# Performance work log

Measured on AMD Instinct MI355X. Metric: run time of the kernel, lower is better.

The kernel has to match this reference:

```python
import jax, jax.numpy as jnp
import numpy as np

DIM = 96
SHIFT_SIZE = 3
EPS = 1e-5


def conv1x1(x, w, b):
    # x: [B,C,H,W], w: [O,C], b: [O]
    return jnp.einsum('bchw,oc->bohw', x, w) + b[None, :, None, None]


def group_norm1(x, gamma, beta):
    # GroupNorm with 1 group: normalize over (C,H,W) per sample
    mean = jnp.mean(x, axis=(1, 2, 3), keepdims=True)
    var = jnp.var(x, axis=(1, 2, 3), keepdims=True)
    xn = (x - mean) * jax.lax.rsqrt(var + EPS)
    return xn * gamma[None, :, None, None] + beta[None, :, None, None]


def axial_shift(x, shift_size, axis, sign=1):
    # pad -> chunk channels -> roll each chunk -> cat -> narrow (zero-fill shift)
    B, C, H, W = x.shape
    p = shift_size // 2
    xp = jnp.pad(x, ((0, 0), (0, 0), (p, p), (p, p)))
    chunks = jnp.split(xp, shift_size, axis=1)
    rolled = [jnp.roll(c, sign * s, axis=axis) for c, s in zip(chunks, range(-p, p + 1))]
    xc = jnp.concatenate(rolled, axis=1)
    return xc[:, :, p:p + H, p:p + W]


def setup_inputs() -> dict:
    key = jax.random.key(0)
    ks = jax.random.split(key, 13)
    B, C, H, W = 4, DIM, 256, 256
    s = 1.0 / np.sqrt(C)
    inp = {
        'x': jax.random.normal(ks[0], (B, C, H, W), jnp.float32),
        'w1': jax.random.uniform(ks[1], (C, C), jnp.float32, -s, s),
        'b1': jax.random.uniform(ks[2], (C,), jnp.float32, -s, s),
        'w21': jax.random.uniform(ks[3], (C, C), jnp.float32, -s, s),
        'b21': jax.random.uniform(ks[4], (C,), jnp.float32, -s, s),
        'w22': jax.random.uniform(ks[5], (C, C), jnp.float32, -s, s),
        'b22': jax.random.uniform(ks[6], (C,), jnp.float32, -s, s),
        'w3': jax.random.uniform(ks[7], (C, C), jnp.float32, -s, s),
        'b3': jax.random.uniform(ks[8], (C,), jnp.float32, -s, s),
        'gn1_w': jnp.ones((C,), jnp.float32),
        'gn1_b': jnp.zeros((C,), jnp.float32),
        'gn2_w': jnp.ones((C,), jnp.float32),
        'gn2_b': jnp.zeros((C,), jnp.float32),
    }
    return inp


def reference(x, w1, b1, w21, b21, w22, b22, w3, b3, gn1_w, gn1_b, gn2_w, gn2_b):
    gelu = lambda t: jax.nn.gelu(t, approximate=False)  # torch nn.GELU default (erf)
    x = gelu(group_norm1(conv1x1(x, w1, b1), gn1_w, gn1_b))
    x_lr = axial_shift(x, SHIFT_SIZE, axis=3)
    x_l_diag = axial_shift(x_lr, SHIFT_SIZE, axis=2)
    x_td = axial_shift(x, SHIFT_SIZE, axis=2)
    x_r_diag = axial_shift(x_td, SHIFT_SIZE, axis=3, sign=-1)
    out = (gelu(conv1x1(x_lr, w21, b21)) + gelu(conv1x1(x_l_diag, w21, b21))
           + gelu(conv1x1(x_td, w22, b22)) + gelu(conv1x1(x_r_diag, w22, b22)))
    out = group_norm1(out, gn2_w, gn2_b)
    return conv1x1(out, w3, b3)
```

## Files before the change

### kernel.cpp

```cpp
#include <hip/hip_runtime.h>
#include <hip/hip_bf16.h>
#include <math.h>


#define B_ 4
#define C_ 96
#define H_ 256
#define W_ 256
#define NPIX (H_ * W_)
#define GN_N ((float)(C_ * NPIX))
#define CPAD 104

#define HT 8
#define WT 16
#define HHT (HT + 2)
#define HWT (WT + 2)
#define HALO_PX (HHT * HWT)
#define GR_PX 12
#define ROW_GR (HWT * GR_PX)
#define TOT_GR (HHT * ROW_GR)

typedef __attribute__((ext_vector_type(4))) float f32x4;
typedef __attribute__((ext_vector_type(8))) short short8;
typedef __attribute__((ext_vector_type(2))) unsigned int uint2v;

__device__ __forceinline__ unsigned short f2bf(float v) {
    unsigned int u = __float_as_uint(v);
    unsigned int r = (u + 0x7FFFu + ((u >> 16) & 1u)) >> 16;
    return (unsigned short)r;
}
__device__ __forceinline__ float bf2f(unsigned short u) {
    return __uint_as_float(((unsigned int)u) << 16);
}

__device__ __forceinline__ float gelu_f(float v) {
    float t = fmaf(v * v, 0.07135481627f, 1.5957691216f);
    float e = __expf(v * t);
    float r = __builtin_amdgcn_rcpf(e + 1.0f);
    return v - v * r;
}

__device__ __forceinline__ float waveReduceSum(float v) {
#pragma unroll
    for (int off = 32; off > 0; off >>= 1) v += __shfl_down(v, off);
    return v;
}

__device__ __forceinline__ f32x4 mfma16(short8 a, short8 b, f32x4 c) {
    return __builtin_amdgcn_mfma_f32_16x16x32_bf16(a, b, c, 0, 0, 0);
}

__global__ void k0_prep(const float* __restrict__ w1, const float* __restrict__ w21,
                        const float* __restrict__ w22, const float* __restrict__ w3,
                        unsigned short* __restrict__ wb, float* __restrict__ stats) {
    int t = blockIdx.x * 256 + threadIdx.x;
    if (blockIdx.x == 0 && threadIdx.x < 16) stats[threadIdx.x] = 0.f;
    if (t >= 4 * C_ * C_) return;
    int m = t / (C_ * C_);
    int r = t - m * (C_ * C_);
    const float* src = (m == 0) ? w1 : (m == 1) ? w21 : (m == 2) ? w22 : w3;
    wb[t] = f2bf(src[r]);
}

__global__ __launch_bounds__(256, 3) void k1_conv1(
    const float* __restrict__ x, const unsigned short* __restrict__ w1b,
    const float* __restrict__ b1, unsigned short* __restrict__ ap,
    float* __restrict__ stats) {
    __shared__ unsigned short xs[256 * CPAD];
    __shared__ float red[8];
    int tid = threadIdx.x;
    int b = blockIdx.x >> 8;
    int h = blockIdx.x & 255;
    int pix0 = h << 8;
    size_t xbase = (size_t)b * C_ * NPIX + pix0 + tid;
    int lb = tid * CPAD;
#pragma unroll
    for (int c0 = 0; c0 < C_; c0 += 8) {
        short8 pk;
#pragma unroll
        for (int j = 0; j < 8; ++j)
            pk[j] = (short)f2bf(x[xbase + (size_t)(c0 + j) * NPIX]);
        *reinterpret_cast<short8*>(&xs[lb + c0]) = pk;
    }
    __syncthreads();
    int l = tid & 63, wv = tid >> 6;
    int bx = l & 15, q = l >> 4, cl = q * 8;
    short8 bfr[4][3];
#pragma unroll
    for (int nf = 0; nf < 4; ++nf) {
        int p = (4 * wv + nf) * 16 + bx;
#pragma unroll
        for (int kb = 0; kb < 3; ++kb)
            bfr[nf][kb] = *reinterpret_cast<const short8*>(&xs[p * CPAD + kb * 32 + cl]);
    }
    unsigned int* xsu = reinterpret_cast<unsigned int*>(xs);
    float ls = 0.f, lsq = 0.f;
    for (int mt = 0; mt < 6; ++mt) {
        int m0 = mt * 16;
        const unsigned short* wp = w1b + (m0 + bx) * C_ + cl;
        short8 af[3];
#pragma unroll
        for (int kb = 0; kb < 3; ++kb)
            af[kb] = *reinterpret_cast<const short8*>(wp + kb * 32);
        f32x4 acc[4];
#pragma unroll
        for (int nf = 0; nf < 4; ++nf) acc[nf] = (f32x4){0.f, 0.f, 0.f, 0.f};
#pragma unroll
        for (int nf = 0; nf < 4; ++nf)
#pragma unroll
            for (int kb = 0; kb < 3; ++kb)
                acc[nf] = mfma16(af[kb], bfr[nf][kb], acc[nf]);
        int o = m0 + q * 4;
        float b0 = b1[o], b1v = b1[o + 1], b2v = b1[o + 2], b3v = b1[o + 3];
#pragma unroll
        for (int nf = 0; nf < 4; ++nf) {
            int p = (4 * wv + nf) * 16 + bx;
            float y0 = acc[nf][0] + b0, y1v = acc[nf][1] + b1v;
            float y2 = acc[nf][2] + b2v, y3 = acc[nf][3] + b3v;
            ls += y0 + y1v + y2 + y3;
            lsq += y0 * y0 + y1v * y1v + y2 * y2 + y3 * y3;
            xsu[p * (CPAD / 2) + (o >> 1)] =
                (unsigned int)f2bf(y0) | ((unsigned int)f2bf(y1v) << 16);
            xsu[p * (CPAD / 2) + (o >> 1) + 1] =
                (unsigned int)f2bf(y2) | ((unsigned int)f2bf(y3) << 16);
        }
    }
    __syncthreads();
    size_t abase = (size_t)(b * NPIX + pix0 + tid) * C_;
#pragma unroll
    for (int c0 = 0; c0 < C_; c0 += 8)
        *reinterpret_cast<short8*>(&ap[abase + c0]) =
            *reinterpret_cast<short8*>(&xs[tid * CPAD + c0]);
    ls = waveReduceSum(ls);
    lsq = waveReduceSum(lsq);
    if (l == 0) { red[wv] = ls; red[4 + wv] = lsq; }
    __syncthreads();
    if (tid == 0) {
        atomicAdd(&stats[b], red[0] + red[1] + red[2] + red[3]);
        atomicAdd(&stats[4 + b], red[4] + red[5] + red[6] + red[7]);
    }
}

__global__ void k2_fin(float* stats, int so, int dof) {
    int t = threadIdx.x;
    if (t < 4) {
        float mean = stats[so + t] / GN_N;
        float var = stats[so + 4 + t] / GN_N - mean * mean;
        stats[dof + t] = mean;
        stats[dof + 4 + t] = rsqrtf(var + 1e-5f);
    }
}

__global__ __launch_bounds__(256, 4) void k3_main(
    const unsigned short* __restrict__ ap,
    const unsigned short* __restrict__ w21b, const float* __restrict__ b21,
    const unsigned short* __restrict__ w22b, const float* __restrict__ b22,
    const float* __restrict__ gn1w, const float* __restrict__ gn1b,
    unsigned short* __restrict__ zb, float* __restrict__ stats) {
    __shared__ unsigned short as_t[HALO_PX * CPAD];
    __shared__ float red[8];
    __shared__ float scs[C_], offs[C_];
    int tid = threadIdx.x;
    int wseg = blockIdx.x & 15;
    int hseg = (blockIdx.x >> 4) & 31;
    int b = blockIdx.x >> 9;
    int l = tid & 63, wv = tid >> 6;
    int h0 = hseg * HT, w0 = wseg * WT;
    float m1 = stats[16 + b], r1 = stats[20 + b];
    if (tid < C_) {
        float sc = r1 * gn1w[tid];
        scs[tid] = sc;
        offs[tid] = gn1b[tid] - m1 * sc;
    }
    __syncthreads();
    for (int g = tid; g < TOT_GR; g += 256) {
        int row = g / ROW_GR;
        int rem = g - row * ROW_GR;
        int p = rem / GR_PX;
        int cgr = rem - p * GR_PX;
        int hh = h0 - 1 + row, ww = w0 - 1 + p;
        bool valid = ((unsigned)hh < (unsigned)H_) && ((unsigned)ww < (unsigned)W_);
        int hc = valid ? hh : 0, wc = valid ? ww : 0;
        short8 raw = *reinterpret_cast<const short8*>(
            &ap[(size_t)(b * NPIX + hc * W_ + wc) * C_ + cgr * 8]);
        short8 pk;
#pragma unroll
        for (int j = 0; j < 8; ++j) {
            int c = cgr * 8 + j;
            float f = bf2f((unsigned short)raw[j]);
            float gv = gelu_f(fmaf(f, scs[c], offs[c]));
            pk[j] = valid ? (short)f2bf(gv) : (short)0;
        }
        *reinterpret_cast<short8*>(&as_t[(row * HWT + p) * CPAD + cgr * 8]) = pk;
    }
    __syncthreads();
    int bx = l & 15, q = l >> 4, cl = q * 8;
    int Xb = (bx + 1) * CPAD + cl;
#define FR(R, dx, kb) (*reinterpret_cast<const short8*>( \
        &as_t[((R)*HWT + (dx)) * CPAD + Xb + (kb)*32]))
    float ls = 0.f, lsq = 0.f;
#pragma unroll
    for (int nf = 0; nf < 2; ++nf) {
        int r = 2 * wv + nf;
        short8 f0a = FR(r + 1, 1, 0), f0b = FR(r + 2, 1, 0);
        short8 f0c = FR(r + 2, 0, 0), f0d = FR(r + 2, -1, 0);
        short8 fC = FR(r + 1, 0, 1);
        short8 f2a = FR(r + 1, -1, 2), f2b = FR(r, -1, 2);
        short8 f2c = FR(r, 0, 2), f2d = FR(r, 1, 2);
        size_t zpix = (size_t)(b * NPIX + (h0 + r) * W_ + w0 + bx) * C_;
        for (int mt = 0; mt < 6; ++mt) {
            int m0 = mt * 16;
            const unsigned short* wpa = w21b + (m0 + bx) * C_ + cl;
            const unsigned short* wpb = w22b + (m0 + bx) * C_ + cl;
            short8 aA0 = *reinterpret_cast<const short8*>(wpa);
            short8 aA1 = *reinterpret_cast<const short8*>(wpa + 32);
            short8 aA2 = *reinterpret_cast<const short8*>(wpa + 64);
            short8 aB0 = *reinterpret_cast<const short8*>(wpb);
            short8 aB1 = *reinterpret_cast<const short8*>(wpb + 32);
            short8 aB2 = *reinterpret_cast<const short8*>(wpb + 64);
            f32x4 a0 = (f32x4){0.f, 0.f, 0.f, 0.f}, a1 = a0, a2 = a0, a3 = a0;
            a0 = mfma16(aA0, f0a, a0);
            a1 = mfma16(aA0, f0b, a1);
            a2 = mfma16(aB0, f0c, a2);
            a3 = mfma16(aB0, f0d, a3);
            a0 = mfma16(aA1, fC, a0);
            a1 = mfma16(aA1, fC, a1);
            a2 = mfma16(aB1, fC, a2);
            a3 = mfma16(aB1, fC, a3);
            a0 = mfma16(aA2, f2a, a0);
            a1 = mfma16(aA2, f2b, a1);
            a2 = mfma16(aB2, f2c, a2);
            a3 = mfma16(aB2, f2d, a3);
            const f32x4 bb1 = *reinterpret_cast<const f32x4*>(&b21[m0 + q * 4]);
            const f32x4 bb2 = *reinterpret_cast<const f32x4*>(&b22[m0 + q * 4]);
            float zv[4];
#pragma unroll
            for (int rg = 0; rg < 4; ++rg) {
                float z0 = gelu_f(a0[rg] + bb1[rg]) + gelu_f(a1[rg] + bb1[rg]) +
                           gelu_f(a2[rg] + bb2[rg]) + gelu_f(a3[rg] + bb2[rg]);
                zv[rg] = z0;
                ls += z0;
                lsq += z0 * z0;
            }
            uint2v pk;
            pk.x = (unsigned int)f2bf(zv[0]) | ((unsigned int)f2bf(zv[1]) << 16);
            pk.y = (unsigned int)f2bf(zv[2]) | ((unsigned int)f2bf(zv[3]) << 16);
            *reinterpret_cast<uint2v*>(&zb[zpix + m0 + q * 4]) = pk;
        }
    }
#undef FR
    ls = waveReduceSum(ls);
    lsq = waveReduceSum(lsq);
    if (l == 0) { red[wv] = ls; red[4 + wv] = lsq; }
    __syncthreads();
    if (tid == 0) {
        atomicAdd(&stats[8 + b], red[0] + red[1] + red[2] + red[3]);
        atomicAdd(&stats[12 + b], red[4] + red[5] + red[6] + red[7]);
    }
}

__global__ __launch_bounds__(256, 3) void k5_conv3(
    const unsigned short* __restrict__ zb,
    const unsigned short* __restrict__ w3b, const float* __restrict__ b3,
    const float* __restrict__ gn2w, const float* __restrict__ gn2b,
    float* __restrict__ out, const float* __restrict__ stats) {
    __shared__ unsigned short zs[256 * CPAD];
    __shared__ float scs[C_], offs[C_];
    int tid = threadIdx.x;
    int b = blockIdx.x >> 8;
    int pix0 = (blockIdx.x & 255) << 8;
    float m2 = stats[24 + b], r2 = stats[28 + b];
    if (tid < C_) {
        float sc = r2 * gn2w[tid];
        scs[tid] = sc;
        offs[tid] = gn2b[tid] - m2 * sc;
    }
    __syncthreads();
    {
        const short8* src = reinterpret_cast<const short8*>(
            &zb[(size_t)(b * NPIX + pix0 + tid) * C_]);
        int lb = tid * CPAD;
#pragma unroll
        for (int i = 0; i < 12; ++i) {
            short8 v = src[i];
            short8 pk;
#pragma unroll
            for (int j = 0; j < 8; ++j) {
                int c = i * 8 + j;
                pk[j] = (short)f2bf(fmaf(bf2f((unsigned short)v[j]), scs[c], offs[c]));
            }
            *reinterpret_cast<short8*>(&zs[lb + i * 8]) = pk;
        }
    }
    __syncthreads();
    int l = tid & 63, wv = tid >> 6;
    int bx = l & 15, q = l >> 4, cl = q * 8;
    short8 bfr[4][3];
#pragma unroll
    for (int nf = 0; nf < 4; ++nf) {
        int p = (4 * wv + nf) * 16 + bx;
#pragma unroll
        for (int kb = 0; kb < 3; ++kb)
            bfr[nf][kb] = *reinterpret_cast<const short8*>(&zs[p * CPAD + kb * 32 + cl]);
    }
    for (int mt = 0; mt < 6; ++mt) {
        int m0 = mt * 16;
        const unsigned short* wp = w3b + (m0 + bx) * C_ + cl;
        short8 af[3];
#pragma unroll
        for (int kb = 0; kb < 3; ++kb)
            af[kb] = *reinterpret_cast<const short8*>(wp + kb * 32);
        f32x4 acc[4];
#pragma unroll
        for (int nf = 0; nf < 4; ++nf) acc[nf] = (f32x4){0.f, 0.f, 0.f, 0.f};
#pragma unroll
        for (int nf = 0; nf < 4; ++nf)
#pragma unroll
            for (int kb = 0; kb < 3; ++kb)
                acc[nf] = mfma16(af[kb], bfr[nf][kb], acc[nf]);
        int o = m0 + q * 4;
        float b0 = b3[o], b1v = b3[o + 1], b2v = b3[o + 2], b3v = b3[o + 3];
#pragma unroll
        for (int nf = 0; nf < 4; ++nf) {
            int p = pix0 + (4 * wv + nf) * 16 + bx;
            size_t ob0 = (size_t)(b * C_ + o) * NPIX + p;
            out[ob0] = acc[nf][0] + b0;
            out[ob0 + NPIX] = acc[nf][1] + b1v;
            out[ob0 + 2 * NPIX] = acc[nf][2] + b2v;
            out[ob0 + 3 * NPIX] = acc[nf][3] + b3v;
        }
    }
}

extern "C" void kernel_launch(void* const* d_in, const int* in_sizes, int n_in,
                              void* d_out, int out_size, void* d_ws, size_t ws_size,
                              hipStream_t stream) {
    const float* x = (const float*)d_in[0];
    const float* w1 = (const float*)d_in[1];
    const float* b1 = (const float*)d_in[2];
    const float* w21 = (const float*)d_in[3];
    const float* b21 = (const float*)d_in[4];
    const float* w22 = (const float*)d_in[5];
    const float* b22 = (const float*)d_in[6];
    const float* w3 = (const float*)d_in[7];
    const float* b3 = (const float*)d_in[8];
    const float* gn1w = (const float*)d_in[9];
    const float* gn1b = (const float*)d_in[10];
    const float* gn2w = (const float*)d_in[11];
    const float* gn2b = (const float*)d_in[12];
    float* out = (float*)d_out;
    char* ws = (char*)d_ws;

    const size_t NB = (size_t)B_ * NPIX * C_ * sizeof(unsigned short);
    unsigned short* ap = (unsigned short*)ws;
    unsigned short* zb = (unsigned short*)(ws + NB);
    float* stats = (float*)(ws + 2 * NB);
    unsigned short* wb = (unsigned short*)(ws + 2 * NB + 128);
    unsigned short* w1b = wb;
    unsigned short* w21b = wb + C_ * C_;
    unsigned short* w22b = wb + 2 * C_ * C_;
    unsigned short* w3b = wb + 3 * C_ * C_;

    hipLaunchKernelGGL(k0_prep, dim3(144), dim3(256), 0, stream,
                       w1, w21, w22, w3, wb, stats);
    hipLaunchKernelGGL(k1_conv1, dim3(1024), dim3(256), 0, stream, x, w1b, b1, ap, stats);
    hipLaunchKernelGGL(k2_fin, dim3(1), dim3(64), 0, stream, stats, 0, 16);
    hipLaunchKernelGGL(k3_main, dim3(2048), dim3(256), 0, stream,
                       ap, w21b, b21, w22b, b22, gn1w, gn1b, zb, stats);
    hipLaunchKernelGGL(k2_fin, dim3(1), dim3(64), 0, stream, stats, 8, 24);
    hipLaunchKernelGGL(k5_conv3, dim3(1024), dim3(256), 0, stream,
                       zb, w3b, b3, gn2w, gn2b, out, stats);
}
```

Before: 170.1 us.

## Split GN1+GELU into own pass, drop LDS halo, fold GN2 into conv3 weights

GroupNorm1 affine plus GELU moves out of the shifted-conv kernel into a separate in-place pass over the activation buffer. The main kernel then reads its shifted fragments straight from global memory with per-load bounds masking instead of staging a halo tile in LDS. That removes the halo recompute of GELU and the LDS footprint, but costs an extra full read/write pass over the activations. GroupNorm2 is folded into per-batch conv3 weights and biases by a tiny kernel, so conv3 loads B fragments directly without LDS normalization. GELU now uses exp2 with pre-scaled constants.

```diff
diff --git a/kernel.cpp b/kernel.cpp
--- a/kernel.cpp
+++ b/kernel.cpp
@@ -11,15 +11,6 @@
 #define GN_N ((float)(C_ * NPIX))
 #define CPAD 104
 
-#define HT 8
-#define WT 16
-#define HHT (HT + 2)
-#define HWT (WT + 2)
-#define HALO_PX (HHT * HWT)
-#define GR_PX 12
-#define ROW_GR (HWT * GR_PX)
-#define TOT_GR (HHT * ROW_GR)
-
 typedef __attribute__((ext_vector_type(4))) float f32x4;
 typedef __attribute__((ext_vector_type(8))) short short8;
 typedef __attribute__((ext_vector_type(2))) unsigned int uint2v;
@@ -34,8 +25,8 @@
 }
 
 __device__ __forceinline__ float gelu_f(float v) {
-    float t = fmaf(v * v, 0.07135481627f, 1.5957691216f);
-    float e = __expf(v * t);
+    float t = fmaf(v * v, 0.1029433f, 2.3021178f);
+    float e = __builtin_amdgcn_exp2f(v * t);
     float r = __builtin_amdgcn_rcpf(e + 1.0f);
     return v - v * r;
 }
@@ -48,6 +39,16 @@
 
 __device__ __forceinline__ f32x4 mfma16(short8 a, short8 b, f32x4 c) {
     return __builtin_amdgcn_mfma_f32_16x16x32_bf16(a, b, c, 0, 0, 0);
+}
+
+__device__ __forceinline__ short8 lfrag(const unsigned short* __restrict__ base,
+                                        int hh, int ww, int ch) {
+    const short8 z = (short8){0, 0, 0, 0, 0, 0, 0, 0};
+    if ((unsigned)hh >= (unsigned)H_) return z;
+    int wc = ww < 0 ? 0 : (ww > W_ - 1 ? W_ - 1 : ww);
+    short8 f = *reinterpret_cast<const short8*>(
+        &base[(size_t)((hh << 8) + wc) * C_ + ch]);
+    return (ww == wc) ? f : z;
 }
 
 __global__ void k0_prep(const float* __restrict__ w1, const float* __restrict__ w21,
@@ -151,21 +152,13 @@
     }
 }
 
-__global__ __launch_bounds__(256, 4) void k3_main(
-    const unsigned short* __restrict__ ap,
-    const unsigned short* __restrict__ w21b, const float* __restrict__ b21,
-    const unsigned short* __restrict__ w22b, const float* __restrict__ b22,
-    const float* __restrict__ gn1w, const float* __restrict__ gn1b,
-    unsigned short* __restrict__ zb, float* __restrict__ stats) {
-    __shared__ unsigned short as_t[HALO_PX * CPAD];
-    __shared__ float red[8];
+__global__ __launch_bounds__(256) void k2b_gelu(
+    unsigned short* __restrict__ ap, const float* __restrict__ gn1w,
+    const float* __restrict__ gn1b, const float* __restrict__ stats) {
     __shared__ float scs[C_], offs[C_];
     int tid = threadIdx.x;
-    int wseg = blockIdx.x & 15;
-    int hseg = (blockIdx.x >> 4) & 31;
-    int b = blockIdx.x >> 9;
-    int l = tid & 63, wv = tid >> 6;
-    int h0 = hseg * HT, w0 = wseg * WT;
+    int b = blockIdx.x >> 8;
+    int pix = ((blockIdx.x & 255) << 8) + tid;
     float m1 = stats[16 + b], r1 = stats[20 + b];
     if (tid < C_) {
         float sc = r1 * gn1w[tid];
@@ -173,82 +166,86 @@
         offs[tid] = gn1b[tid] - m1 * sc;
     }
     __syncthreads();
-    for (int g = tid; g < TOT_GR; g += 256) {
-        int row = g / ROW_GR;
-        int rem = g - row * ROW_GR;
-        int p = rem / GR_PX;
-        int cgr = rem - p * GR_PX;
-        int hh = h0 - 1 + row, ww = w0 - 1 + p;
-        bool valid = ((unsigned)hh < (unsigned)H_) && ((unsigned)ww < (unsigned)W_);
-        int hc = valid ? hh : 0, wc = valid ? ww : 0;
-        short8 raw = *reinterpret_cast<const short8*>(
-            &ap[(size_t)(b * NPIX + hc * W_ + wc) * C_ + cgr * 8]);
+    size_t base = (size_t)(b * NPIX + pix) * C_;
+#pragma unroll
+    for (int i = 0; i < 12; ++i) {
+        short8 v = *reinterpret_cast<const short8*>(&ap[base + i * 8]);
         short8 pk;
 #pragma unroll
         for (int j = 0; j < 8; ++j) {
-            int c = cgr * 8 + j;
-            float f = bf2f((unsigned short)raw[j]);
-            float gv = gelu_f(fmaf(f, scs[c], offs[c]));
-            pk[j] = valid ? (short)f2bf(gv) : (short)0;
-        }
-        *reinterpret_cast<short8*>(&as_t[(row * HWT + p) * CPAD + cgr * 8]) = pk;
-    }
-    __syncthreads();
+            int c = i * 8 + j;
+            pk[j] = (short)f2bf(gelu_f(fmaf(bf2f((unsigned short)v[j]), scs[c], offs[c])));
+        }
+        *reinterpret_cast<short8*>(&ap[base + i * 8]) = pk;
+    }
+}
+
+__global__ __launch_bounds__(256, 4) void k3_main(
+    const unsigned short* __restrict__ ag,
+    const unsigned short* __restrict__ w21b, const float* __restrict__ b21,
+    const unsigned short* __restrict__ w22b, const float* __restrict__ b22,
+    unsigned short* __restrict__ zb, float* __restrict__ stats) {
+    __shared__ float red[8];
+    int tid = threadIdx.x;
+    int l = tid & 63, wv = tid >> 6;
+    int wseg = blockIdx.x & 15;
+    int hseg = (blockIdx.x >> 4) & 63;
+    int b = blockIdx.x >> 10;
+    int h = hseg * 4 + wv;
     int bx = l & 15, q = l >> 4, cl = q * 8;
-    int Xb = (bx + 1) * CPAD + cl;
-#define FR(R, dx, kb) (*reinterpret_cast<const short8*>( \
-        &as_t[((R)*HWT + (dx)) * CPAD + Xb + (kb)*32]))
+    int w = (wseg << 4) + bx;
+    const unsigned short* base = ag + (size_t)b * NPIX * C_;
+    short8 f0a = lfrag(base, h, w + 1, cl);
+    short8 f0b = lfrag(base, h + 1, w + 1, cl);
+    short8 f0c = lfrag(base, h + 1, w, cl);
+    short8 f0d = lfrag(base, h + 1, w - 1, cl);
+    short8 fC = lfrag(base, h, w, 32 + cl);
+    short8 f2a = lfrag(base, h, w - 1, 64 + cl);
+    short8 f2b = lfrag(base, h - 1, w - 1, 64 + cl);
+    short8 f2c = lfrag(base, h - 1, w, 64 + cl);
+    short8 f2d = lfrag(base, h - 1, w + 1, 64 + cl);
     float ls = 0.f, lsq = 0.f;
-#pragma unroll
-    for (int nf = 0; nf < 2; ++nf) {
-        int r = 2 * wv + nf;
-        short8 f0a = FR(r + 1, 1, 0), f0b = FR(r + 2, 1, 0);
-        short8 f0c = FR(r + 2, 0, 0), f0d = FR(r + 2, -1, 0);
-        short8 fC = FR(r + 1, 0, 1);
-        short8 f2a = FR(r + 1, -1, 2), f2b = FR(r, -1, 2);
-        short8 f2c = FR(r, 0, 2), f2d = FR(r, 1, 2);
-        size_t zpix = (size_t)(b * NPIX + (h0 + r) * W_ + w0 + bx) * C_;
-        for (int mt = 0; mt < 6; ++mt) {
-            int m0 = mt * 16;
-            const unsigned short* wpa = w21b + (m0 + bx) * C_ + cl;
-            const unsigned short* wpb = w22b + (m0 + bx) * C_ + cl;
-            short8 aA0 = *reinterpret_cast<const short8*>(wpa);
-            short8 aA1 = *reinterpret_cast<const short8*>(wpa + 32);
-            short8 aA2 = *reinterpret_cast<const short8*>(wpa + 64);
-            short8 aB0 = *reinterpret_cast<const short8*>(wpb);
-            short8 aB1 = *reinterpret_cast<const short8*>(wpb + 32);
-            short8 aB2 = *reinterpret_cast<const short8*>(wpb + 64);
-            f32x4 a0 = (f32x4){0.f, 0.f, 0.f, 0.f}, a1 = a0, a2 = a0, a3 = a0;
-            a0 = mfma16(aA0, f0a, a0);
-            a1 = mfma16(aA0, f0b, a1);
-            a2 = mfma16(aB0, f0c, a2);
-            a3 = mfma16(aB0, f0d, a3);
-            a0 = mfma16(aA1, fC, a0);
-            a1 = mfma16(aA1, fC, a1);
-            a2 = mfma16(aB1, fC, a2);
-            a3 = mfma16(aB1, fC, a3);
-            a0 = mfma16(aA2, f2a, a0);
-            a1 = mfma16(aA2, f2b, a1);
-            a2 = mfma16(aB2, f2c, a2);
-            a3 = mfma16(aB2, f2d, a3);
-            const f32x4 bb1 = *reinterpret_cast<const f32x4*>(&b21[m0 + q * 4]);
-            const f32x4 bb2 = *reinterpret_cast<const f32x4*>(&b22[m0 + q * 4]);
-            float zv[4];
-#pragma unroll
-            for (int rg = 0; rg < 4; ++rg) {
-                float z0 = gelu_f(a0[rg] + bb1[rg]) + gelu_f(a1[rg] + bb1[rg]) +
-                           gelu_f(a2[rg] + bb2[rg]) + gelu_f(a3[rg] + bb2[rg]);
-                zv[rg] = z0;
-                ls += z0;
-                lsq += z0 * z0;
-            }
-            uint2v pk;
-            pk.x = (unsigned int)f2bf(zv[0]) | ((unsigned int)f2bf(zv[1]) << 16);
-            pk.y = (unsigned int)f2bf(zv[2]) | ((unsigned int)f2bf(zv[3]) << 16);
-            *reinterpret_cast<uint2v*>(&zb[zpix + m0 + q * 4]) = pk;
-        }
-    }
-#undef FR
+    size_t zpix = ((size_t)b * NPIX + (h << 8) + w) * C_;
+#pragma unroll 1
+    for (int mt = 0; mt < 6; ++mt) {
+        int m0 = mt * 16;
+        const unsigned short* wpa = w21b + (m0 + bx) * C_ + cl;
+        const unsigned short* wpb = w22b + (m0 + bx) * C_ + cl;
+        short8 aA0 = *reinterpret_cast<const short8*>(wpa);
+        short8 aA1 = *reinterpret_cast<const short8*>(wpa + 32);
+        short8 aA2 = *reinterpret_cast<const short8*>(wpa + 64);
+        short8 aB0 = *reinterpret_cast<const short8*>(wpb);
+        short8 aB1 = *reinterpret_cast<const short8*>(wpb + 32);
+        short8 aB2 = *reinterpret_cast<const short8*>(wpb + 64);
+        f32x4 a0 = (f32x4){0.f, 0.f, 0.f, 0.f}, a1 = a0, a2 = a0, a3 = a0;
+        a0 = mfma16(aA0, f0a, a0);
+        a1 = mfma16(aA0, f0b, a1);
+        a2 = mfma16(aB0, f0c, a2);
+        a3 = mfma16(aB0, f0d, a3);
+        a0 = mfma16(aA1, fC, a0);
+        a1 = mfma16(aA1, fC, a1);
+        a2 = mfma16(aB1, fC, a2);
+        a3 = mfma16(aB1, fC, a3);
+        a0 = mfma16(aA2, f2a, a0);
+        a1 = mfma16(aA2, f2b, a1);
+        a2 = mfma16(aB2, f2c, a2);
+        a3 = mfma16(aB2, f2d, a3);
+        const f32x4 bb1 = *reinterpret_cast<const f32x4*>(&b21[m0 + q * 4]);
+        const f32x4 bb2 = *reinterpret_cast<const f32x4*>(&b22[m0 + q * 4]);
+        float zv[4];
+#pragma unroll
+        for (int rg = 0; rg < 4; ++rg) {
+            float z0 = gelu_f(a0[rg] + bb1[rg]) + gelu_f(a1[rg] + bb1[rg]) +
+                       gelu_f(a2[rg] + bb2[rg]) + gelu_f(a3[rg] + bb2[rg]);
+            zv[rg] = z0;
+            ls += z0;
+            lsq += z0 * z0;
+        }
+        uint2v pk;
+        pk.x = (unsigned int)f2bf(zv[0]) | ((unsigned int)f2bf(zv[1]) << 16);
+        pk.y = (unsigned int)f2bf(zv[2]) | ((unsigned int)f2bf(zv[3]) << 16);
+        *reinterpret_cast<uint2v*>(&zb[zpix + m0 + q * 4]) = pk;
+    }
     ls = waveReduceSum(ls);
     lsq = waveReduceSum(lsq);
     if (l == 0) { red[wv] = ls; red[4 + wv] = lsq; }
@@ -259,67 +256,65 @@
     }
 }
 
-__global__ __launch_bounds__(256, 3) void k5_conv3(
+__global__ void k4b_fold(const float* __restrict__ w3, const float* __restrict__ b3,
+                         const float* __restrict__ gn2w, const float* __restrict__ gn2b,
+                         const float* __restrict__ stats,
+                         unsigned short* __restrict__ w3p, float* __restrict__ b3p) {
+    int b = blockIdx.x;
+    int o = threadIdx.x;
+    float mean = stats[8 + b] / GN_N;
+    float var = stats[12 + b] / GN_N - mean * mean;
+    float r2 = rsqrtf(var + 1e-5f);
+    float acc = 0.f;
+    for (int c = 0; c < C_; ++c) {
+        float sc = r2 * gn2w[c];
+        float off = gn2b[c] - mean * sc;
+        float wv = w3[o * C_ + c];
+        acc = fmaf(wv, off, acc);
+        w3p[((size_t)b * C_ + o) * C_ + c] = f2bf(wv * sc);
+    }
+    b3p[b * C_ + o] = acc + b3[o];
+}
+
+__global__ __launch_bounds__(256, 4) void k5_conv3(
     const unsigned short* __restrict__ zb,
-    const unsigned short* __restrict__ w3b, const float* __restrict__ b3,
-    const float* __restrict__ gn2w, const float* __restrict__ gn2b,
-    float* __restrict__ out, const float* __restrict__ stats) {
-    __shared__ unsigned short zs[256 * CPAD];
-    __shared__ float scs[C_], offs[C_];
+    const unsigned short* __restrict__ w3p, const float* __restrict__ b3p,
+    float* __restrict__ out) {
     int tid = threadIdx.x;
     int b = blockIdx.x >> 8;
     int pix0 = (blockIdx.x & 255) << 8;
-    float m2 = stats[24 + b], r2 = stats[28 + b];
-    if (tid < C_) {
-        float sc = r2 * gn2w[tid];
-        scs[tid] = sc;
-        offs[tid] = gn2b[tid] - m2 * sc;
-    }
-    __syncthreads();
-    {
-        const short8* src = reinterpret_cast<const short8*>(
-            &zb[(size_t)(b * NPIX + pix0 + tid) * C_]);
-        int lb = tid * CPAD;
-#pragma unroll
-        for (int i = 0; i < 12; ++i) {
-            short8 v = src[i];
-            short8 pk;
-#pragma unroll
-            for (int j = 0; j < 8; ++j) {
-                int c = i * 8 + j;
-                pk[j] = (short)f2bf(fmaf(bf2f((unsigned short)v[j]), scs[c], offs[c]));
-            }
-            *reinterpret_cast<short8*>(&zs[lb + i * 8]) = pk;
-        }
-    }
-    __syncthreads();
     int l = tid & 63, wv = tid >> 6;
     int bx = l & 15, q = l >> 4, cl = q * 8;
+    const unsigned short* zp = zb + (size_t)(b * NPIX + pix0) * C_;
     short8 bfr[4][3];
 #pragma unroll
     for (int nf = 0; nf < 4; ++nf) {
         int p = (4 * wv + nf) * 16 + bx;
 #pragma unroll
         for (int kb = 0; kb < 3; ++kb)
-            bfr[nf][kb] = *reinterpret_cast<const short8*>(&zs[p * CPAD + kb * 32 + cl]);
-    }
+            bfr[nf][kb] = *reinterpret_cast<const short8*>(
+                &zp[(size_t)p * C_ + kb * 32 + cl]);
+    }
+    const unsigned short* wbase = w3p + (size_t)b * C_ * C_;
+    const float* bb = b3p + b * C_;
+#pragma unroll 1
     for (int mt = 0; mt < 6; ++mt) {
         int m0 = mt * 16;
-        const unsigned short* wp = w3b + (m0 + bx) * C_ + cl;
-        short8 af[3];
-#pragma unroll
-        for (int kb = 0; kb < 3; ++kb)
-            af[kb] = *reinterpret_cast<const short8*>(wp + kb * 32);
+        const unsigned short* wp = wbase + (m0 + bx) * C_ + cl;
+        short8 af0 = *reinterpret_cast<const short8*>(wp);
+        short8 af1 = *reinterpret_cast<const short8*>(wp + 32);
+        short8 af2 = *reinterpret_cast<const short8*>(wp + 64);
         f32x4 acc[4];
 #pragma unroll
         for (int nf = 0; nf < 4; ++nf) acc[nf] = (f32x4){0.f, 0.f, 0.f, 0.f};
 #pragma unroll
-        for (int nf = 0; nf < 4; ++nf)
-#pragma unroll
-            for (int kb = 0; kb < 3; ++kb)
-                acc[nf] = mfma16(af[kb], bfr[nf][kb], acc[nf]);
+        for (int nf = 0; nf < 4; ++nf) {
+            acc[nf] = mfma16(af0, bfr[nf][0], acc[nf]);
+            acc[nf] = mfma16(af1, bfr[nf][1], acc[nf]);
+            acc[nf] = mfma16(af2, bfr[nf][2], acc[nf]);
+        }
         int o = m0 + q * 4;
-        float b0 = b3[o], b1v = b3[o + 1], b2v = b3[o + 2], b3v = b3[o + 3];
+        float b0 = bb[o], b1v = bb[o + 1], b2v = bb[o + 2], b3v = bb[o + 3];
 #pragma unroll
         for (int nf = 0; nf < 4; ++nf) {
             int p = pix0 + (4 * wv + nf) * 16 + bx;
@@ -359,15 +354,19 @@
     unsigned short* w1b = wb;
     unsigned short* w21b = wb + C_ * C_;
     unsigned short* w22b = wb + 2 * C_ * C_;
-    unsigned short* w3b = wb + 3 * C_ * C_;
+    unsigned short* w3p = wb + 4 * C_ * C_;
+    float* b3p = (float*)(w3p + B_ * C_ * C_);
 
     hipLaunchKernelGGL(k0_prep, dim3(144), dim3(256), 0, stream,
                        w1, w21, w22, w3, wb, stats);
     hipLaunchKernelGGL(k1_conv1, dim3(1024), dim3(256), 0, stream, x, w1b, b1, ap, stats);
     hipLaunchKernelGGL(k2_fin, dim3(1), dim3(64), 0, stream, stats, 0, 16);
-    hipLaunchKernelGGL(k3_main, dim3(2048), dim3(256), 0, stream,
-                       ap, w21b, b21, w22b, b22, gn1w, gn1b, zb, stats);
-    hipLaunchKernelGGL(k2_fin, dim3(1), dim3(64), 0, stream, stats, 8, 24);
+    hipLaunchKernelGGL(k2b_gelu, dim3(1024), dim3(256), 0, stream,
+                       ap, gn1w, gn1b, stats);
+    hipLaunchKernelGGL(k3_main, dim3(4096), dim3(256), 0, stream,
+                       ap, w21b, b21, w22b, b22, zb, stats);
+    hipLaunchKernelGGL(k4b_fold, dim3(B_), dim3(C_), 0, stream,
+                       w3, b3, gn2w, gn2b, stats, w3p, b3p);
     hipLaunchKernelGGL(k5_conv3, dim3(1024), dim3(256), 0, stream,
-                       zb, w3b, b3, gn2w, gn2b, out, stats);
-}
+                       zb, w3p, b3p, out);
+}
```

After: 255.4 us. 50.1% more time.

## Fold GroupNorm2 affine into per-batch conv3 weights and seed MFMA with bias

Applied to the files above, without the earlier changes.

Adds a small kernel that folds the second GroupNorm's per-sample scale and offset into a per-batch bf16 copy of w3 and an adjusted bias. The conv3 kernel then copies the z tile straight into LDS without the per-element normalize and re-round, and that kernel replaces the stats finalize launch. The conv2 stage now initializes its MFMA accumulators with the bias instead of adding it afterwards. GELU calls exp2 directly with constants prescaled by log2(e). Folding the scale into weights changes where bf16 rounding happens, which can shift accuracy slightly, and the fold kernel runs serially with only a few blocks.

```diff
diff --git a/kernel.cpp b/kernel.cpp
--- a/kernel.cpp
+++ b/kernel.cpp
@@ -34,8 +34,8 @@
 }
 
 __device__ __forceinline__ float gelu_f(float v) {
-    float t = fmaf(v * v, 0.07135481627f, 1.5957691216f);
-    float e = __expf(v * t);
+    float t = fmaf(v * v, 0.1029433f, 2.3021178f);
+    float e = __builtin_amdgcn_exp2f(v * t);
     float r = __builtin_amdgcn_rcpf(e + 1.0f);
     return v - v * r;
 }
@@ -218,7 +218,9 @@
             short8 aB0 = *reinterpret_cast<const short8*>(wpb);
             short8 aB1 = *reinterpret_cast<const short8*>(wpb + 32);
             short8 aB2 = *reinterpret_cast<const short8*>(wpb + 64);
-            f32x4 a0 = (f32x4){0.f, 0.f, 0.f, 0.f}, a1 = a0, a2 = a0, a3 = a0;
+            const f32x4 bb1 = *reinterpret_cast<const f32x4*>(&b21[m0 + q * 4]);
+            const f32x4 bb2 = *reinterpret_cast<const f32x4*>(&b22[m0 + q * 4]);
+            f32x4 a0 = bb1, a1 = bb1, a2 = bb2, a3 = bb2;
             a0 = mfma16(aA0, f0a, a0);
             a1 = mfma16(aA0, f0b, a1);
             a2 = mfma16(aB0, f0c, a2);
@@ -231,13 +233,11 @@
             a1 = mfma16(aA2, f2b, a1);
             a2 = mfma16(aB2, f2c, a2);
             a3 = mfma16(aB2, f2d, a3);
-            const f32x4 bb1 = *reinterpret_cast<const f32x4*>(&b21[m0 + q * 4]);
-            const f32x4 bb2 = *reinterpret_cast<const f32x4*>(&b22[m0 + q * 4]);
             float zv[4];
 #pragma unroll
             for (int rg = 0; rg < 4; ++rg) {
-                float z0 = gelu_f(a0[rg] + bb1[rg]) + gelu_f(a1[rg] + bb1[rg]) +
-                           gelu_f(a2[rg] + bb2[rg]) + gelu_f(a3[rg] + bb2[rg]);
+                float z0 = gelu_f(a0[rg]) + gelu_f(a1[rg]) +
+                           gelu_f(a2[rg]) + gelu_f(a3[rg]);
                 zv[rg] = z0;
                 ls += z0;
                 lsq += z0 * z0;
@@ -259,38 +259,41 @@
     }
 }
 
+__global__ void k4b_fold(const float* __restrict__ w3, const float* __restrict__ b3,
+                         const float* __restrict__ gn2w, const float* __restrict__ gn2b,
+                         const float* __restrict__ stats,
+                         unsigned short* __restrict__ w3p, float* __restrict__ b3p) {
+    int b = blockIdx.x;
+    int o = threadIdx.x;
+    float mean = stats[8 + b] / GN_N;
+    float var = stats[12 + b] / GN_N - mean * mean;
+    float r2 = rsqrtf(var + 1e-5f);
+    float acc = 0.f;
+    for (int c = 0; c < C_; ++c) {
+        float sc = r2 * gn2w[c];
+        float off = gn2b[c] - mean * sc;
+        float wv = w3[o * C_ + c];
+        acc = fmaf(wv, off, acc);
+        w3p[((size_t)b * C_ + o) * C_ + c] = f2bf(wv * sc);
+    }
+    b3p[b * C_ + o] = acc + b3[o];
+}
+
 __global__ __launch_bounds__(256, 3) void k5_conv3(
     const unsigned short* __restrict__ zb,
-    const unsigned short* __restrict__ w3b, const float* __restrict__ b3,
-    const float* __restrict__ gn2w, const float* __restrict__ gn2b,
-    float* __restrict__ out, const float* __restrict__ stats) {
+    const unsigned short* __restrict__ w3p, const float* __restrict__ b3p,
+    float* __restrict__ out) {
     __shared__ unsigned short zs[256 * CPAD];
-    __shared__ float scs[C_], offs[C_];
     int tid = threadIdx.x;
     int b = blockIdx.x >> 8;
     int pix0 = (blockIdx.x & 255) << 8;
-    float m2 = stats[24 + b], r2 = stats[28 + b];
-    if (tid < C_) {
-        float sc = r2 * gn2w[tid];
-        scs[tid] = sc;
-        offs[tid] = gn2b[tid] - m2 * sc;
-    }
-    __syncthreads();
     {
         const short8* src = reinterpret_cast<const short8*>(
             &zb[(size_t)(b * NPIX + pix0 + tid) * C_]);
         int lb = tid * CPAD;
 #pragma unroll
-        for (int i = 0; i < 12; ++i) {
-            short8 v = src[i];
-            short8 pk;
-#pragma unroll
-            for (int j = 0; j < 8; ++j) {
-                int c = i * 8 + j;
-                pk[j] = (short)f2bf(fmaf(bf2f((unsigned short)v[j]), scs[c], offs[c]));
-            }
-            *reinterpret_cast<short8*>(&zs[lb + i * 8]) = pk;
-        }
+        for (int i = 0; i < 12; ++i)
+            *reinterpret_cast<short8*>(&zs[lb + i * 8]) = src[i];
     }
     __syncthreads();
     int l = tid & 63, wv = tid >> 6;
@@ -303,23 +306,25 @@
         for (int kb = 0; kb < 3; ++kb)
             bfr[nf][kb] = *reinterpret_cast<const short8*>(&zs[p * CPAD + kb * 32 + cl]);
     }
+    const unsigned short* wbase = w3p + (size_t)b * C_ * C_;
+    const float* bb = b3p + b * C_;
     for (int mt = 0; mt < 6; ++mt) {
         int m0 = mt * 16;
-        const unsigned short* wp = w3b + (m0 + bx) * C_ + cl;
-        short8 af[3];
-#pragma unroll
-        for (int kb = 0; kb < 3; ++kb)
-            af[kb] = *reinterpret_cast<const short8*>(wp + kb * 32);
+        const unsigned short* wp = wbase + (m0 + bx) * C_ + cl;
+        short8 af0 = *reinterpret_cast<const short8*>(wp);
+        short8 af1 = *reinterpret_cast<const short8*>(wp + 32);
+        short8 af2 = *reinterpret_cast<const short8*>(wp + 64);
         f32x4 acc[4];
 #pragma unroll
         for (int nf = 0; nf < 4; ++nf) acc[nf] = (f32x4){0.f, 0.f, 0.f, 0.f};
 #pragma unroll
-        for (int nf = 0; nf < 4; ++nf)
-#pragma unroll
-            for (int kb = 0; kb < 3; ++kb)
-                acc[nf] = mfma16(af[kb], bfr[nf][kb], acc[nf]);
+        for (int nf = 0; nf < 4; ++nf) {
+            acc[nf] = mfma16(af0, bfr[nf][0], acc[nf]);
+            acc[nf] = mfma16(af1, bfr[nf][1], acc[nf]);
+            acc[nf] = mfma16(af2, bfr[nf][2], acc[nf]);
+        }
         int o = m0 + q * 4;
-        float b0 = b3[o], b1v = b3[o + 1], b2v = b3[o + 2], b3v = b3[o + 3];
+        float b0 = bb[o], b1v = bb[o + 1], b2v = bb[o + 2], b3v = bb[o + 3];
 #pragma unroll
         for (int nf = 0; nf < 4; ++nf) {
             int p = pix0 + (4 * wv + nf) * 16 + bx;
@@ -359,7 +364,8 @@
     unsigned short* w1b = wb;
     unsigned short* w21b = wb + C_ * C_;
     unsigned short* w22b = wb + 2 * C_ * C_;
-    unsigned short* w3b = wb + 3 * C_ * C_;
+    unsigned short* w3p = wb + 4 * C_ * C_;
+    float* b3p = (float*)(w3p + B_ * C_ * C_);
 
     hipLaunchKernelGGL(k0_prep, dim3(144), dim3(256), 0, stream,
                        w1, w21, w22, w3, wb, stats);
@@ -367,7 +373,8 @@
     hipLaunchKernelGGL(k2_fin, dim3(1), dim3(64), 0, stream, stats, 0, 16);
     hipLaunchKernelGGL(k3_main, dim3(2048), dim3(256), 0, stream,
                        ap, w21b, b21, w22b, b22, gn1w, gn1b, zb, stats);
-    hipLaunchKernelGGL(k2_fin, dim3(1), dim3(64), 0, stream, stats, 8, 24);
+    hipLaunchKernelGGL(k4b_fold, dim3(B_), dim3(C_), 0, stream,
+                       w3, b3, gn2w, gn2b, stats, w3p, b3p);
     hipLaunchKernelGGL(k5_conv3, dim3(1024), dim3(256), 0, stream,
-                       zb, w3b, b3, gn2w, gn2b, out, stats);
-}
+                       zb, w3p, b3p, out);
+}
```

Result: slower. 176.2 us (+3.6%).
